# Kernel tuning notes

Hardware: AMD Instinct MI355X
Metric: run time of the kernel (lower is better)

The kernel has to match this reference:

```python
import jax, jax.numpy as jnp
import numpy as np

B = 4096
D = 1024
N = 9000000
TEMPERATURE = 0.1
GAMMA = 0.8
ALPHA = 0.5
EPS = 1e-14


def setup_inputs() -> dict:
    key = jax.random.key(0)
    k1, k2, k3, k4, k5 = jax.random.split(key, 5)
    zis = jax.random.normal(k1, (B, D), dtype=jnp.float32)
    zjs = jax.random.normal(k2, (B, D), dtype=jnp.float32)
    s_I = jax.random.uniform(k3, (N,), dtype=jnp.float32)
    s_T = jax.random.uniform(k4, (N,), dtype=jnp.float32)
    b_I = jnp.zeros((N,), dtype=jnp.float32)
    b_T = jnp.zeros((N,), dtype=jnp.float32)
    ids = jax.random.randint(k5, (B,), 0, N, dtype=jnp.int64 if jax.config.jax_enable_x64 else jnp.int32)
    return {"zis": zis, "zjs": zjs, "s_I": s_I, "s_T": s_T, "b_I": b_I, "b_T": b_T, "ids": ids}


def reference(zis, zjs, s_I, s_T, b_I, b_T, ids):
    sg = jax.lax.stop_gradient
    # L2 normalize embeddings (norm=True path)
    zis = zis / jnp.linalg.norm(zis, axis=1, keepdims=True)
    zjs = zjs / jnp.linalg.norm(zjs, axis=1, keepdims=True)
    sim = jnp.einsum('id,jd->ij', zis, zjs)            # [B, B]
    diag = jnp.diagonal(sim)                            # [B]
    image_diffs = sim - diag[:, None]
    text_diffs = sim - diag[None, :]
    # detached, temperature-scaled diffs (torch .clone().detach_())
    idd = sg(image_diffs) / TEMPERATURE
    tdd = sg(text_diffs) / TEMPERATURE
    # online max tracking (per-id running max b)
    old_b_I = b_I[ids]                                  # gather [B]
    new_b_I = jnp.maximum(idd.max(axis=1), old_b_I)
    old_b_T = b_T[ids]
    new_b_T = jnp.maximum(tdd.max(axis=0), old_b_T)
    mask_neg = 1.0 - jnp.eye(B, dtype=sim.dtype)
    exp_image_diffs = jnp.exp(idd - new_b_I[:, None]) * mask_neg
    exp_text_diffs = jnp.exp(tdd - new_b_T[None, :]) * mask_neg
    g_I = exp_image_diffs.sum(axis=1) / (B - 1)         # [B]
    g_T = exp_text_diffs.sum(axis=0) / (B - 1)          # [B]
    # EMA of softmax denominator with rescaling for new max
    s_I_new = (1.0 - GAMMA) * s_I[ids] * jnp.exp(old_b_I - new_b_I) + GAMMA * g_I
    s_T_new = (1.0 - GAMMA) * s_T[ids] * jnp.exp(old_b_T - new_b_T) + GAMMA * g_T
    # state writes (side effects in torch; computed for fidelity)
    b_I = b_I.at[ids].set(new_b_I)
    b_T = b_T.at[ids].set(new_b_T)
    s_I = s_I.at[ids].set(s_I_new)
    s_T = s_T.at[ids].set(s_T_new)
    s_I_c = jnp.maximum(s_I_new, EPS)
    s_T_c = jnp.maximum(s_T_new, EPS)
    weights_image = exp_image_diffs / s_I_c[:, None]    # detached weights
    weights_text = exp_text_diffs / s_T_c[None, :]
    image_loss = (weights_image * image_diffs).sum(axis=1) / (B - 1)
    text_loss = (weights_text * text_diffs).sum(axis=0) / (B - 1)
    total_loss = ALPHA * image_loss.mean() + (1.0 - ALPHA) * text_loss.mean()
    return total_loss
```

## Files before the change

### kernel.cpp

```cpp
#include <hip/hip_runtime.h>
#include <stdint.h>

#define B_ 4096
#define D_ 1024
#define BM 256
#define BN 128
#define BK 64
#define NT 16
#define TINV 10.0f
#define LOG2E 1.4426950408889634f
#define KE (TINV * LOG2E)
#define INV_BM1 (1.0f / 4095.0f)

typedef float f32x4 __attribute__((ext_vector_type(4)));

__device__ __forceinline__ unsigned short f2bf(float x) {
  uint32_t b = __float_as_uint(x);
  b += 0x7FFF + ((b >> 16) & 1);
  return (unsigned short)(b >> 16);
}

__device__ __forceinline__ uint8_t f2e4m3(float x) {
  uint32_t u = __float_as_uint(x);
  uint32_t s = (u >> 24) & 0x80;
  int e = (int)((u >> 23) & 0xFF) - 127;
  uint32_t m = u & 0x7FFFFF;
  if (e >= -6) {
    uint32_t mant = m >> 20;
    uint32_t rest = m & 0xFFFFF;
    uint32_t rnd = (rest > 0x80000u) || (rest == 0x80000u && (mant & 1));
    mant += rnd;
    uint32_t exp4 = (uint32_t)(e + 7);
    if (mant == 8) { mant = 0; exp4++; }
    return (uint8_t)(s | (exp4 << 3) | mant);
  } else {
    uint32_t M = 0x800000u | m;
    int sh = 20 + (-6 - e);
    if (sh > 31) return (uint8_t)s;
    uint32_t mant = M >> sh;
    uint32_t rest = M & ((1u << sh) - 1);
    uint32_t half = 1u << (sh - 1);
    uint32_t rnd = (rest > half) || (rest == half && (mant & 1));
    mant += rnd;
    return (uint8_t)(s | mant);
  }
}

__device__ __forceinline__ void gload16(const void* g, void* l) {
  __builtin_amdgcn_global_load_lds(
      (const __attribute__((address_space(1))) uint32_t*)g,
      (__attribute__((address_space(3))) uint32_t*)l, 16, 0, 0);
}

__global__ __launch_bounds__(256) void k_normalize(const float* __restrict__ zis,
                                                   const float* __restrict__ zjs,
                                                   uint8_t* __restrict__ Aq,
                                                   uint8_t* __restrict__ Bq) {
  int r = blockIdx.x;
  const float* src;
  uint8_t* dst;
  if (r < B_) { src = zis + (size_t)r * D_; dst = Aq + (size_t)r * D_; }
  else        { src = zjs + (size_t)(r - B_) * D_; dst = Bq + (size_t)(r - B_) * D_; }
  int t = threadIdx.x;
  float4 v = reinterpret_cast<const float4*>(src)[t];
  float ss = v.x*v.x + v.y*v.y + v.z*v.z + v.w*v.w;
  #pragma unroll
  for (int o = 32; o >= 1; o >>= 1) ss += __shfl_down(ss, o);
  __shared__ float red[4];
  if ((t & 63) == 0) red[t >> 6] = ss;
  __syncthreads();
  float sc = rsqrtf(red[0] + red[1] + red[2] + red[3]);
  uchar4 o4;
  o4.x = f2e4m3(v.x * sc); o4.y = f2e4m3(v.y * sc);
  o4.z = f2e4m3(v.z * sc); o4.w = f2e4m3(v.w * sc);
  reinterpret_cast<uchar4*>(dst)[t] = o4;
}

__global__ __launch_bounds__(512, 4) void k_gemm(const uint8_t* __restrict__ A,
                                                 const uint8_t* __restrict__ B,
                                                 unsigned short* __restrict__ C,
                                                 float* __restrict__ diagp) {
  __shared__ uint8_t lds[3][24576];
  const int tid = threadIdx.x;
  const int wid = tid >> 6;
  const int lane = tid & 63;
  const int wm = wid >> 1;
  const int wn = wid & 1;
  const int bRow = blockIdx.y * BM;
  const int bCol = blockIdx.x * BN;
  const uint8_t* Ag = A + (size_t)bRow * D_;
  const uint8_t* Bg = B + (size_t)bCol * D_;

  const int lrow = lane >> 2;
  const int scol = ((lane & 3) * 16) ^ (lane & 48);
  const size_t soA0 = (size_t)(wid * 32 + lrow) * D_ + scol;
  const size_t soA1 = (size_t)(wid * 32 + 16 + lrow) * D_ + scol;
  const size_t soB  = (size_t)(wid * 16 + lrow) * D_ + scol;

  const int fr = lane & 15;
  const int kq = lane >> 4;
  const int sx = (fr & 12) << 2;

  f32x4 acc[4][4] = {};

#define STAGE(T, SL) {                                                        \
    const uint8_t* gA_ = Ag + (size_t)(T) * BK;                               \
    const uint8_t* gB_ = Bg + (size_t)(T) * BK;                               \
    gload16(gA_ + soA0, &lds[SL][(2 * wid + 0) * 1024]);                      \
    gload16(gA_ + soA1, &lds[SL][(2 * wid + 1) * 1024]);                      \
    gload16(gB_ + soB,  &lds[SL][16384 + wid * 1024]); }

  STAGE(0, 0); STAGE(1, 1);
  asm volatile("s_waitcnt vmcnt(3)" ::: "memory");
  __builtin_amdgcn_sched_barrier(0);
  __builtin_amdgcn_s_barrier();
  __builtin_amdgcn_sched_barrier(0);

  int sl = 0, sl2 = 2;
  for (int t = 0; t < NT; ++t) {
    const uint8_t* Lb = lds[sl];
    long long a8[4][2], b8[4][2];
    #pragma unroll
    for (int m = 0; m < 4; ++m) {
      const uint8_t* rp = &Lb[(wm * 64 + m * 16 + fr) * 64];
      a8[m][0] = *reinterpret_cast<const long long*>(&rp[(kq * 8) ^ sx]);
      a8[m][1] = *reinterpret_cast<const long long*>(&rp[(32 + kq * 8) ^ sx]);
    }
    #pragma unroll
    for (int n = 0; n < 4; ++n) {
      const uint8_t* rp = &Lb[16384 + (wn * 64 + n * 16 + fr) * 64];
      b8[n][0] = *reinterpret_cast<const long long*>(&rp[(kq * 8) ^ sx]);
      b8[n][1] = *reinterpret_cast<const long long*>(&rp[(32 + kq * 8) ^ sx]);
    }
    if (t + 2 < NT) STAGE(t + 2, sl2);
    __builtin_amdgcn_s_setprio(1);
    #pragma unroll
    for (int m = 0; m < 4; ++m)
      #pragma unroll
      for (int n = 0; n < 4; ++n) {
        acc[m][n] = __builtin_amdgcn_mfma_f32_16x16x32_fp8_fp8(
            a8[m][0], b8[n][0], acc[m][n], 0, 0, 0);
        acc[m][n] = __builtin_amdgcn_mfma_f32_16x16x32_fp8_fp8(
            a8[m][1], b8[n][1], acc[m][n], 0, 0, 0);
      }
    __builtin_amdgcn_s_setprio(0);
    if (t < NT - 2) {
      asm volatile("s_waitcnt vmcnt(3)" ::: "memory");
    } else if (t == NT - 2) {
      asm volatile("s_waitcnt vmcnt(0)" ::: "memory");
    }
    __builtin_amdgcn_sched_barrier(0);
    if (t < NT - 1) {
      __builtin_amdgcn_s_barrier();
      __builtin_amdgcn_sched_barrier(0);
    }
    sl = (sl == 2) ? 0 : sl + 1;
    sl2 = (sl2 == 2) ? 0 : sl2 + 1;
  }

  const int fr4 = kq * 4;
  #pragma unroll
  for (int m = 0; m < 4; ++m)
    #pragma unroll
    for (int n = 0; n < 4; ++n)
      #pragma unroll
      for (int q = 0; q < 4; ++q) {
        float v = acc[m][n][q];
        int rg = bRow + wm * 64 + m * 16 + fr4 + q;
        int cg = bCol + wn * 64 + n * 16 + fr;
        if (rg == cg) diagp[rg] = v;
        float p = __shfl_xor(v, 1);
        if (!(lane & 1)) {
          uint32_t u = (uint32_t)f2bf(v) | ((uint32_t)f2bf(p) << 16);
          *reinterpret_cast<uint32_t*>(&C[(size_t)rg * B_ + cg]) = u;
        }
      }
#undef STAGE
}

__global__ __launch_bounds__(1024) void k_fused(const unsigned short* __restrict__ sim,
    const float* __restrict__ diag,
    const float* __restrict__ bI, const float* __restrict__ sI,
    const int* __restrict__ ids,
    float* __restrict__ LI, float* __restrict__ cmax_p,
    float* __restrict__ cE_p, float* __restrict__ cE2_p) {
  const int i0 = blockIdx.x * 16;
  const int t = threadIdx.x;
  const int w = t >> 6, lane = t & 63;
  __shared__ float rowPart[16][16][3];

  float cmax[4], cE[4], cE2[4];
  #pragma unroll
  for (int k = 0; k < 4; ++k) { cmax[k] = -3.4e38f; cE[k] = 0.f; cE2[k] = 0.f; }

  for (int r = 0; r < 16; ++r) {
    const unsigned short* sp = sim + (size_t)(i0 + r) * B_ + t * 4;
    uint2 u0 = *reinterpret_cast<const uint2*>(sp);
    float x[4];
    x[0] = __uint_as_float(u0.x << 16); x[1] = __uint_as_float(u0.x & 0xffff0000u);
    x[2] = __uint_as_float(u0.y << 16); x[3] = __uint_as_float(u0.y & 0xffff0000u);
    float rmx = -3.4e38f, rE = 0.f, rE2 = 0.f;
    #pragma unroll
    for (int k = 0; k < 4; ++k) {
      float e = exp2f(x[k] * KE);
      rmx = fmaxf(rmx, x[k]);
      rE += e;
      rE2 = fmaf(e, x[k], rE2);
      cmax[k] = fmaxf(cmax[k], x[k]);
      cE[k] += e;
      cE2[k] = fmaf(e, x[k], cE2[k]);
    }
    #pragma unroll
    for (int o = 32; o >= 1; o >>= 1) {
      rmx = fmaxf(rmx, __shfl_down(rmx, o));
      rE += __shfl_down(rE, o);
      rE2 += __shfl_down(rE2, o);
    }
    if (lane == 0) { rowPart[r][w][0] = rmx; rowPart[r][w][1] = rE; rowPart[r][w][2] = rE2; }
  }
  __syncthreads();
  if (t < 16) {
    int i = i0 + t;
    float mx = -3.4e38f, E = 0.f, E2 = 0.f;
    #pragma unroll
    for (int k = 0; k < 16; ++k) {
      mx = fmaxf(mx, rowPart[t][k][0]);
      E += rowPart[t][k][1];
      E2 += rowPart[t][k][2];
    }
    float dg = diag[i];
    float ed = exp2f(dg * KE);
    int id = ids[i];
    float oldb = bI[id];
    float newb = fmaxf((mx - dg) * TINV, oldb);
    float sc = exp2f(-(dg * TINV + newb) * LOG2E);
    float S1 = (E - ed) * sc;
    float S2 = (E2 - dg * E) * sc;
    float g = S1 * INV_BM1;
    float sn = 0.2f * sI[id] * exp2f((oldb - newb) * LOG2E) + 0.8f * g;
    LI[i] = S2 / fmaxf(sn, 1e-14f) * INV_BM1;
  }
  size_t base = (size_t)blockIdx.x * B_ + t * 4;
  #pragma unroll
  for (int k = 0; k < 4; ++k) {
    cmax_p[base + k] = cmax[k];
    cE_p[base + k]   = cE[k];
    cE2_p[base + k]  = cE2[k];
  }
}

__global__ __launch_bounds__(256) void k_colred(
    const float* __restrict__ diag,
    const float* __restrict__ cmax_p, const float* __restrict__ cE_p,
    const float* __restrict__ cE2_p,
    const float* __restrict__ bT, const float* __restrict__ sT,
    const int* __restrict__ ids, const float* __restrict__ LI,
    float* __restrict__ partial) {
  const int t = threadIdx.x;
  const int cidx = t >> 5;
  const int sub = t & 31;
  const int j = blockIdx.x * 8 + cidx;
  float mx = -3.4e38f, E = 0.f, E2 = 0.f;
  #pragma unroll
  for (int k = 0; k < 8; ++k) {
    size_t o = (size_t)(sub + 32 * k) * B_ + j;
    mx = fmaxf(mx, cmax_p[o]);
    E += cE_p[o];
    E2 += cE2_p[o];
  }
  #pragma unroll
  for (int o = 16; o >= 1; o >>= 1) {
    mx = fmaxf(mx, __shfl_down(mx, o, 32));
    E += __shfl_down(E, o, 32);
    E2 += __shfl_down(E2, o, 32);
  }
  __shared__ float red[8];
  if (sub == 0) {
    float dg = diag[j];
    float ed = exp2f(dg * KE);
    int id = ids[j];
    float oldb = bT[id];
    float newb = fmaxf((mx - dg) * TINV, oldb);
    float sc = exp2f(-(dg * TINV + newb) * LOG2E);
    float S1 = (E - ed) * sc;
    float S2 = (E2 - dg * E) * sc;
    float g = S1 * INV_BM1;
    float sn = 0.2f * sT[id] * exp2f((oldb - newb) * LOG2E) + 0.8f * g;
    float lt = S2 / fmaxf(sn, 1e-14f) * INV_BM1;
    red[cidx] = (0.5f * LI[j] + 0.5f * lt) * (1.0f / (float)B_);
  }
  __syncthreads();
  if (t == 0) {
    float s = 0.f;
    #pragma unroll
    for (int k = 0; k < 8; ++k) s += red[k];
    partial[blockIdx.x] = s;
  }
}

__global__ void k_final2(const float* __restrict__ partial, float* __restrict__ out) {
  int t = threadIdx.x;
  float v = partial[t];
  #pragma unroll
  for (int o = 32; o >= 1; o >>= 1) v += __shfl_down(v, o);
  __shared__ float red[8];
  if ((t & 63) == 0) red[t >> 6] = v;
  __syncthreads();
  if (t == 0) {
    float s = 0.f;
    #pragma unroll
    for (int k = 0; k < 8; ++k) s += red[k];
    out[0] = s;
  }
}

extern "C" void kernel_launch(void* const* d_in, const int* in_sizes, int n_in,
                              void* d_out, int out_size, void* d_ws, size_t ws_size,
                              hipStream_t stream) {
  const float* zis = (const float*)d_in[0];
  const float* zjs = (const float*)d_in[1];
  const float* s_I = (const float*)d_in[2];
  const float* s_T = (const float*)d_in[3];
  const float* b_I = (const float*)d_in[4];
  const float* b_T = (const float*)d_in[5];
  const int*   ids = (const int*)d_in[6];

  char* ws = (char*)d_ws;
  size_t off = 0;
  auto alloc = [&](size_t bytes) -> void* {
    void* p = ws + off;
    off = (off + bytes + 255) & ~(size_t)255;
    return p;
  };
  uint8_t* Aq = (uint8_t*)alloc((size_t)B_ * D_);
  uint8_t* Bq = (uint8_t*)alloc((size_t)B_ * D_);
  unsigned short* sim = (unsigned short*)alloc((size_t)B_ * B_ * 2);
  float* diag   = (float*)alloc(B_ * 4);
  float* cmax_p = (float*)alloc((size_t)256 * B_ * 4);
  float* cE_p   = (float*)alloc((size_t)256 * B_ * 4);
  float* cE2_p  = (float*)alloc((size_t)256 * B_ * 4);
  float* LI     = (float*)alloc(B_ * 4);
  float* partial = (float*)alloc(512 * 4);

  k_normalize<<<2 * B_, 256, 0, stream>>>(zis, zjs, Aq, Bq);
  k_gemm<<<dim3(B_ / BN, B_ / BM), 512, 0, stream>>>(Aq, Bq, sim, diag);
  k_fused<<<256, 1024, 0, stream>>>(sim, diag, b_I, s_I, ids, LI, cmax_p, cE_p, cE2_p);
  k_colred<<<512, 256, 0, stream>>>(diag, cmax_p, cE_p, cE2_p, b_T, s_T, ids, LI, partial);
  k_final2<<<1, 512, 0, stream>>>(partial, (float*)d_out);
}
```

Measured before the change: 80.31 us.

## Use scaled 16x16x128 FP8 MFMA with a 128x128 tile and 4-stage pipeline

The similarity GEMM switches from pairs of 16x16x32 FP8 MFMAs to the gfx950 scaled 16x16x128 f8f6f4 MFMA, with unit scales, so each instruction covers two 64-wide K tiles. The block tile drops from 256x128 with 512 threads to 128x128 with 256 threads. The LDS ring grows to four stages, loading two K tiles per iteration with an extra barrier before buffers are refilled. The aim is more MFMA throughput per instruction and better occupancy. The cost is larger register operands and more blocks that re-read A and B.

```diff
diff --git a/kernel.cpp b/kernel.cpp
--- a/kernel.cpp
+++ b/kernel.cpp
@@ -3,7 +3,7 @@
 
 #define B_ 4096
 #define D_ 1024
-#define BM 256
+#define BM 128
 #define BN 128
 #define BK 64
 #define NT 16
@@ -11,8 +11,10 @@
 #define LOG2E 1.4426950408889634f
 #define KE (TINV * LOG2E)
 #define INV_BM1 (1.0f / 4095.0f)
+#define SC1 0x7F7F7F7F
 
 typedef float f32x4 __attribute__((ext_vector_type(4)));
+typedef int   i32x8 __attribute__((ext_vector_type(8)));
 
 __device__ __forceinline__ unsigned short f2bf(float x) {
   uint32_t b = __float_as_uint(x);
@@ -76,11 +78,11 @@
   reinterpret_cast<uchar4*>(dst)[t] = o4;
 }
 
-__global__ __launch_bounds__(512, 4) void k_gemm(const uint8_t* __restrict__ A,
+__global__ __launch_bounds__(256, 2) void k_gemm(const uint8_t* __restrict__ A,
                                                  const uint8_t* __restrict__ B,
                                                  unsigned short* __restrict__ C,
                                                  float* __restrict__ diagp) {
-  __shared__ uint8_t lds[3][24576];
+  __shared__ uint8_t lds[4][16384];
   const int tid = threadIdx.x;
   const int wid = tid >> 6;
   const int lane = tid & 63;
@@ -95,67 +97,79 @@
   const int scol = ((lane & 3) * 16) ^ (lane & 48);
   const size_t soA0 = (size_t)(wid * 32 + lrow) * D_ + scol;
   const size_t soA1 = (size_t)(wid * 32 + 16 + lrow) * D_ + scol;
-  const size_t soB  = (size_t)(wid * 16 + lrow) * D_ + scol;
 
   const int fr = lane & 15;
   const int kq = lane >> 4;
   const int sx = (fr & 12) << 2;
+  const int o0 = (kq * 8) ^ sx;
+  const int o1 = (32 + kq * 8) ^ sx;
 
   f32x4 acc[4][4] = {};
 
 #define STAGE(T, SL) {                                                        \
-    const uint8_t* gA_ = Ag + (size_t)(T) * BK;                               \
-    const uint8_t* gB_ = Bg + (size_t)(T) * BK;                               \
+    const uint8_t* gA_ = A + (size_t)(bRow + 0) * D_ + (size_t)(T) * BK;      \
+    const uint8_t* gB_ = B + (size_t)(bCol + 0) * D_ + (size_t)(T) * BK;      \
     gload16(gA_ + soA0, &lds[SL][(2 * wid + 0) * 1024]);                      \
     gload16(gA_ + soA1, &lds[SL][(2 * wid + 1) * 1024]);                      \
-    gload16(gB_ + soB,  &lds[SL][16384 + wid * 1024]); }
-
-  STAGE(0, 0); STAGE(1, 1);
-  asm volatile("s_waitcnt vmcnt(3)" ::: "memory");
+    gload16(gB_ + soA0, &lds[SL][8192 + (2 * wid + 0) * 1024]);               \
+    gload16(gB_ + soA1, &lds[SL][8192 + (2 * wid + 1) * 1024]); }
+
+  STAGE(0, 0); STAGE(1, 1); STAGE(2, 2); STAGE(3, 3);
+  asm volatile("s_waitcnt vmcnt(8)" ::: "memory");
   __builtin_amdgcn_sched_barrier(0);
   __builtin_amdgcn_s_barrier();
   __builtin_amdgcn_sched_barrier(0);
 
-  int sl = 0, sl2 = 2;
-  for (int t = 0; t < NT; ++t) {
-    const uint8_t* Lb = lds[sl];
-    long long a8[4][2], b8[4][2];
+  for (int i = 0; i < 8; ++i) {
+    const int s0 = (2 * i) & 3, s1 = (2 * i + 1) & 3;
+    const uint8_t* L0 = lds[s0];
+    const uint8_t* L1 = lds[s1];
+    i32x8 av[4], bv[4];
     #pragma unroll
     for (int m = 0; m < 4; ++m) {
-      const uint8_t* rp = &Lb[(wm * 64 + m * 16 + fr) * 64];
-      a8[m][0] = *reinterpret_cast<const long long*>(&rp[(kq * 8) ^ sx]);
-      a8[m][1] = *reinterpret_cast<const long long*>(&rp[(32 + kq * 8) ^ sx]);
+      const uint8_t* r0 = &L0[(wm * 64 + m * 16 + fr) * 64];
+      const uint8_t* r1 = &L1[(wm * 64 + m * 16 + fr) * 64];
+      int2 c0 = *reinterpret_cast<const int2*>(&r0[o0]);
+      int2 c1 = *reinterpret_cast<const int2*>(&r0[o1]);
+      int2 c2 = *reinterpret_cast<const int2*>(&r1[o0]);
+      int2 c3 = *reinterpret_cast<const int2*>(&r1[o1]);
+      av[m][0] = c0.x; av[m][1] = c0.y; av[m][2] = c1.x; av[m][3] = c1.y;
+      av[m][4] = c2.x; av[m][5] = c2.y; av[m][6] = c3.x; av[m][7] = c3.y;
     }
     #pragma unroll
     for (int n = 0; n < 4; ++n) {
-      const uint8_t* rp = &Lb[16384 + (wn * 64 + n * 16 + fr) * 64];
-      b8[n][0] = *reinterpret_cast<const long long*>(&rp[(kq * 8) ^ sx]);
-      b8[n][1] = *reinterpret_cast<const long long*>(&rp[(32 + kq * 8) ^ sx]);
-    }
-    if (t + 2 < NT) STAGE(t + 2, sl2);
+      const uint8_t* r0 = &L0[8192 + (wn * 64 + n * 16 + fr) * 64];
+      const uint8_t* r1 = &L1[8192 + (wn * 64 + n * 16 + fr) * 64];
+      int2 c0 = *reinterpret_cast<const int2*>(&r0[o0]);
+      int2 c1 = *reinterpret_cast<const int2*>(&r0[o1]);
+      int2 c2 = *reinterpret_cast<const int2*>(&r1[o0]);
+      int2 c3 = *reinterpret_cast<const int2*>(&r1[o1]);
+      bv[n][0] = c0.x; bv[n][1] = c0.y; bv[n][2] = c1.x; bv[n][3] = c1.y;
+      bv[n][4] = c2.x; bv[n][5] = c2.y; bv[n][6] = c3.x; bv[n][7] = c3.y;
+    }
+    asm volatile("s_waitcnt lgkmcnt(0)" ::: "memory");
+    __builtin_amdgcn_sched_barrier(0);
+    __builtin_amdgcn_s_barrier();
+    __builtin_amdgcn_sched_barrier(0);
+    if (2 * i + 4 < NT) { STAGE(2 * i + 4, s0); STAGE(2 * i + 5, s1); }
     __builtin_amdgcn_s_setprio(1);
     #pragma unroll
     for (int m = 0; m < 4; ++m)
       #pragma unroll
-      for (int n = 0; n < 4; ++n) {
-        acc[m][n] = __builtin_amdgcn_mfma_f32_16x16x32_fp8_fp8(
-            a8[m][0], b8[n][0], acc[m][n], 0, 0, 0);
-        acc[m][n] = __builtin_amdgcn_mfma_f32_16x16x32_fp8_fp8(
-            a8[m][1], b8[n][1], acc[m][n], 0, 0, 0);
-      }
+      for (int n = 0; n < 4; ++n)
+        acc[m][n] = __builtin_amdgcn_mfma_scale_f32_16x16x128_f8f6f4(
+            av[m], bv[n], acc[m][n], 0, 0, 0, SC1, 0, SC1);
     __builtin_amdgcn_s_setprio(0);
-    if (t < NT - 2) {
-      asm volatile("s_waitcnt vmcnt(3)" ::: "memory");
-    } else if (t == NT - 2) {
+    if (i < 6) {
+      asm volatile("s_waitcnt vmcnt(8)" ::: "memory");
+    } else if (i == 6) {
       asm volatile("s_waitcnt vmcnt(0)" ::: "memory");
     }
     __builtin_amdgcn_sched_barrier(0);
-    if (t < NT - 1) {
+    if (i < 7) {
       __builtin_amdgcn_s_barrier();
       __builtin_amdgcn_sched_barrier(0);
     }
-    sl = (sl == 2) ? 0 : sl + 1;
-    sl2 = (sl2 == 2) ? 0 : sl2 + 1;
   }
 
   const int fr4 = kq * 4;
@@ -343,7 +357,7 @@
   float* partial = (float*)alloc(512 * 4);
 
   k_normalize<<<2 * B_, 256, 0, stream>>>(zis, zjs, Aq, Bq);
-  k_gemm<<<dim3(B_ / BN, B_ / BM), 512, 0, stream>>>(Aq, Bq, sim, diag);
+  k_gemm<<<dim3(B_ / BN, B_ / BM), 256, 0, stream>>>(Aq, Bq, sim, diag);
   k_fused<<<256, 1024, 0, stream>>>(sim, diag, b_I, s_I, ids, LI, cmax_p, cE_p, cE2_p);
   k_colred<<<512, 256, 0, stream>>>(diag, cmax_p, cE_p, cE2_p, b_T, s_T, ids, LI, partial);
   k_final2<<<1, 512, 0, stream>>>(partial, (float*)d_out);
```

Result: slower. 234.9 us (+192.6%).
